# Performance work log

Hardware: AMD Instinct MI355X
Metric: run time of the kernel (lower is better)

The kernel has to match this reference:

```python
import jax, jax.numpy as jnp
import numpy as np

N_NODES = 50000
N_EDGES = 250000
D_IN, D_HID, D_OUT = 768, 256, 2


def _sage_conv(x, src, dst, W_l, b_l, W_r, n_nodes):
    # PyG SAGEConv (aggr='mean', root_weight=True):
    #   out[i] = lin_l(mean_{j in N(i)} x[j]) + lin_r(x[i])
    msg = x[src]  # [E, d] gather of source-node features
    agg = jax.ops.segment_sum(msg, dst, num_segments=n_nodes)
    cnt = jax.ops.segment_sum(jnp.ones((src.shape[0],), x.dtype), dst,
                              num_segments=n_nodes)
    agg = agg / jnp.maximum(cnt, 1.0)[:, None]
    return agg @ W_l.T + b_l + x @ W_r.T


def setup_inputs() -> dict:
    key = jax.random.key(0)
    ks = jax.random.split(key, 7)
    x = jax.random.normal(ks[0], (N_NODES, D_IN), dtype=jnp.float32)
    edge_index = jax.random.randint(ks[1], (2, N_EDGES), 0, N_NODES,
                                    dtype=jnp.int64)
    s1 = 1.0 / np.sqrt(D_IN)
    s2 = 1.0 / np.sqrt(D_HID)
    W1_l = jax.random.uniform(ks[2], (D_HID, D_IN), jnp.float32, -s1, s1)
    W1_r = jax.random.uniform(ks[3], (D_HID, D_IN), jnp.float32, -s1, s1)
    b1 = jnp.zeros((D_HID,), jnp.float32)
    W2_l = jax.random.uniform(ks[4], (D_OUT, D_HID), jnp.float32, -s2, s2)
    W2_r = jax.random.uniform(ks[5], (D_OUT, D_HID), jnp.float32, -s2, s2)
    b2 = jnp.zeros((D_OUT,), jnp.float32)
    return {"x": x, "edge_index": edge_index,
            "W1_l": W1_l, "b1": b1, "W1_r": W1_r,
            "W2_l": W2_l, "b2": b2, "W2_r": W2_r}


def reference(x, edge_index, W1_l, b1, W1_r, W2_l, b2, W2_r):
    src, dst = edge_index[0], edge_index[1]
    n = x.shape[0]
    h = _sage_conv(x, src, dst, W1_l, b1, W1_r, n)
    h = jax.nn.relu(h)
    # dropout is identity in eval mode (deterministic reference)
    out = _sage_conv(h, src, dst, W2_l, b2, W2_r, n)
    return out
```

## Files before the change

kernel.cpp:

```cpp
#include <hip/hip_runtime.h>
#include <stdint.h>


#define D_IN  768
#define D_HID 256
#define N1    512
#define KITERS (D_IN / 32)

typedef __attribute__((ext_vector_type(8))) short short8;
typedef __attribute__((ext_vector_type(4))) float f32x4;

__device__ __forceinline__ void async_copy16(const void* g, void* l) {
  __builtin_amdgcn_global_load_lds(
      (const __attribute__((address_space(1))) unsigned int*)g,
      (__attribute__((address_space(3))) unsigned int*)l,
      16, 0, 0);
}

__device__ __forceinline__ unsigned short f2bf(float f) {
  union { float f; unsigned u; } v; v.f = f;
  unsigned r = v.u + 0x7FFFu + ((v.u >> 16) & 1u);
  return (unsigned short)(r >> 16);
}

__device__ __forceinline__ float bf2f(unsigned short b) {
  union { unsigned u; float f; } v; v.u = ((unsigned)b) << 16;
  return v.f;
}


__global__ void cvtidx_k(const void* __restrict__ eidx,
                         int* __restrict__ src32, int* __restrict__ dst32,
                         int* __restrict__ counts, int E) {
  __shared__ int flag32;
  int tid = threadIdx.x;
  int i = blockIdx.x * 256 + tid;
  unsigned v = (i < E) ? ((const unsigned int*)eidx)[2 * (size_t)i + 1] : 0u;
  unsigned long long any = __ballot(v != 0u);
  if (tid == 0) flag32 = 0;
  __syncthreads();
  if ((tid & 63) == 0 && any) flag32 = 1;
  __syncthreads();
  if (i >= E) return;
  int s, d;
  if (flag32) {
    const int* p = (const int*)eidx;
    s = p[i]; d = p[E + i];
  } else {
    const long long* p = (const long long*)eidx;
    s = (int)p[i]; d = (int)p[E + i];
  }
  src32[i] = s;
  dst32[i] = d;
  atomicAdd(&counts[d], 1);
}

__global__ void scanA_k(const int* __restrict__ counts,
                        int* __restrict__ blockSums, int M) {
  __shared__ int ts[256];
  int b = blockIdx.x, t = threadIdx.x;
  int base = b * 1024 + t * 4;
  int s = 0;
#pragma unroll
  for (int k = 0; k < 4; k++) { int i = base + k; if (i < M) s += counts[i]; }
  ts[t] = s;
  __syncthreads();
  for (int off = 128; off > 0; off >>= 1) {
    if (t < off) ts[t] += ts[t + off];
    __syncthreads();
  }
  if (t == 0) blockSums[b] = ts[0];
}

__global__ void scanC_k(const int* __restrict__ counts,
                        const int* __restrict__ bsums,
                        int* __restrict__ offs, int* __restrict__ cursor,
                        int M, int E, int nb) {
  __shared__ int ts[256];
  __shared__ int bofs;
  int b = blockIdx.x, t = threadIdx.x;
  if (t < 64) {
    int v = (t < nb) ? bsums[t] : 0;
    int orig = v;
#pragma unroll
    for (int off = 1; off < 64; off <<= 1) {
      int u = __shfl_up(v, off);
      if (t >= off) v += u;
    }
    if (t == b) bofs = v - orig;
  }
  int base = b * 1024 + t * 4;
  int v[4]; int s = 0;
#pragma unroll
  for (int k = 0; k < 4; k++) {
    int i = base + k;
    v[k] = (i < M) ? counts[i] : 0;
    s += v[k];
  }
  ts[t] = s;
  __syncthreads();
  for (int off = 1; off < 256; off <<= 1) {
    int x = (t >= off) ? ts[t - off] : 0;
    __syncthreads();
    ts[t] += x;
    __syncthreads();
  }
  int run = bofs + ts[t] - s;
#pragma unroll
  for (int k = 0; k < 4; k++) {
    int i = base + k;
    if (i < M) { offs[i] = run; cursor[i] = run; run += v[k]; }
  }
  if (b == 0 && t == 0) offs[M] = E;
}

__global__ void fill_k(const int* __restrict__ src, const int* __restrict__ dst,
                       int* __restrict__ cursor, int* __restrict__ csr, int E) {
  int i = blockIdx.x * 256 + threadIdx.x;
  if (i >= E) return;
  int pos = atomicAdd(&cursor[dst[i]], 1);
  csr[pos] = src[i];
}


__global__ void cvtw_k(const float* __restrict__ W1l, const float* __restrict__ W1r,
                       unsigned short* __restrict__ wb) {
  int idx = blockIdx.x * 256 + threadIdx.x;
  int total = N1 * (D_IN / 8);
  if (idx >= total) return;
  int row = idx / (D_IN / 8);
  int cpos = (idx % (D_IN / 8)) * 8;
  const float* p = (row < D_HID) ? (W1l + (size_t)row * D_IN + cpos)
                                 : (W1r + (size_t)(row - D_HID) * D_IN + cpos);
  float4 f0 = *(const float4*)p;
  float4 f1 = *(const float4*)(p + 4);
  short8 o;
  o[0] = (short)f2bf(f0.x); o[1] = (short)f2bf(f0.y);
  o[2] = (short)f2bf(f0.z); o[3] = (short)f2bf(f0.w);
  o[4] = (short)f2bf(f1.x); o[5] = (short)f2bf(f1.y);
  o[6] = (short)f2bf(f1.z); o[7] = (short)f2bf(f1.w);
  *(short8*)(wb + (size_t)idx * 8) = o;
}

__global__ __launch_bounds__(256) void gemm_k(
    const float* __restrict__ x,
    const unsigned short* __restrict__ wb,
    unsigned short* __restrict__ Cb, int M) {
  __shared__ unsigned short As[2][128 * 32];
  __shared__ unsigned short Bs[2][128 * 32];
  const int tid  = threadIdx.x;
  const int lane = tid & 63;
  const int wid  = tid >> 6;
  const int wr = wid >> 1, wc = wid & 1;
  const int m0 = blockIdx.y * 128;
  const int n0 = blockIdx.x * 128;
  const int l15  = lane & 15;
  const int quad = lane >> 4;

  const int arow0 = tid >> 2, akg = tid & 3;
  const int arow1 = arow0 + 64;
  const int aswz = akg | ((akg & 1) << 2);
  const float* agp0 = x + (size_t)min(m0 + arow0, M - 1) * D_IN + akg * 8;
  const float* agp1 = x + (size_t)min(m0 + arow1, M - 1) * D_IN + akg * 8;
  const int aoff0 = (arow0 >> 4) * 512 + akg * 128 + ((arow0 & 15) ^ aswz) * 8;
  const int aoff1 = (arow1 >> 4) * 512 + akg * 128 + ((arow1 & 15) ^ aswz) * 8;
  const int pquad = quad | ((quad & 1) << 2);

  const int brow = (tid >> 6) * 16 + (tid & 15);
  const int bcg  = (tid >> 4) & 3;
  const unsigned short* bgp0 = wb + (size_t)(n0 + brow) * D_IN + bcg * 8;
  const unsigned short* bgp1 = wb + (size_t)(n0 + brow + 64) * D_IN + bcg * 8;
  const int boff0 = tid * 8;
  const int boff1 = (tid + 256) * 8;

  f32x4 acc[4][4];
#pragma unroll
  for (int r = 0; r < 4; r++)
#pragma unroll
    for (int c = 0; c < 4; c++) acc[r][c] = (f32x4)0.0f;

  float4 a00 = *(const float4*)(agp0);
  float4 a01 = *(const float4*)(agp0 + 4);
  float4 a10 = *(const float4*)(agp1);
  float4 a11 = *(const float4*)(agp1 + 4);
  async_copy16(bgp0, &Bs[0][boff0]);
  async_copy16(bgp1, &Bs[0][boff1]);

  for (int it = 0; it < KITERS; ++it) {
    const int p = it & 1;
    short8 o0, o1;
    o0[0] = (short)f2bf(a00.x); o0[1] = (short)f2bf(a00.y);
    o0[2] = (short)f2bf(a00.z); o0[3] = (short)f2bf(a00.w);
    o0[4] = (short)f2bf(a01.x); o0[5] = (short)f2bf(a01.y);
    o0[6] = (short)f2bf(a01.z); o0[7] = (short)f2bf(a01.w);
    o1[0] = (short)f2bf(a10.x); o1[1] = (short)f2bf(a10.y);
    o1[2] = (short)f2bf(a10.z); o1[3] = (short)f2bf(a10.w);
    o1[4] = (short)f2bf(a11.x); o1[5] = (short)f2bf(a11.y);
    o1[6] = (short)f2bf(a11.z); o1[7] = (short)f2bf(a11.w);
    *(short8*)&As[p][aoff0] = o0;
    *(short8*)&As[p][aoff1] = o1;

    __syncthreads();

    if (it + 1 < KITERS) {
      const int k1 = (it + 1) * 32;
      a00 = *(const float4*)(agp0 + k1);
      a01 = *(const float4*)(agp0 + k1 + 4);
      a10 = *(const float4*)(agp1 + k1);
      a11 = *(const float4*)(agp1 + k1 + 4);
      async_copy16(bgp0 + k1, &Bs[p ^ 1][boff0]);
      async_copy16(bgp1 + k1, &Bs[p ^ 1][boff1]);
    }

    short8 a[4], b[4];
#pragma unroll
    for (int r = 0; r < 4; r++)
      a[r] = *(const short8*)&As[p][(wr * 4 + r) * 512 + quad * 128 + ((l15 ^ pquad)) * 8];
#pragma unroll
    for (int c = 0; c < 4; c++)
      b[c] = *(const short8*)&Bs[p][(wc * 4 + c) * 512 + quad * 128 + l15 * 8];
#pragma unroll
    for (int r = 0; r < 4; r++)
#pragma unroll
      for (int c = 0; c < 4; c++)
        acc[r][c] = __builtin_amdgcn_mfma_f32_16x16x32_bf16(a[r], b[c], acc[r][c], 0, 0, 0);
  }

  const int crow0 = m0 + wr * 64;
  const int ccol0 = n0 + wc * 64;
#pragma unroll
  for (int r = 0; r < 4; r++)
#pragma unroll
    for (int c = 0; c < 4; c++) {
      int col = ccol0 + c * 16 + l15;
#pragma unroll
      for (int reg = 0; reg < 4; reg++) {
        int row = crow0 + r * 16 + quad * 4 + reg;
        Cb[(size_t)row * N1 + col] = f2bf(acc[r][c][reg]);
      }
    }
}

__global__ void agg_l2_k(const unsigned short* __restrict__ Cb,
                         const int* __restrict__ offs, const int* __restrict__ csr,
                         const float* __restrict__ b1,
                         const float* __restrict__ W2l, const float* __restrict__ W2r,
                         float4* __restrict__ rs, int M) {
  int tid = threadIdx.x;
  int lane = tid & 63;
  int wid = tid >> 6;
  int wave = blockIdx.x * 4 + wid;
  int nw = gridDim.x * 4;
  int c = lane * 4;
  float4 bv  = *(const float4*)(b1 + c);
  float4 wl0 = *(const float4*)(W2l + c);
  float4 wl1 = *(const float4*)(W2l + D_HID + c);
  float4 wr0 = *(const float4*)(W2r + c);
  float4 wr1 = *(const float4*)(W2r + D_HID + c);
  for (int i = wave; i < M; i += nw) {
    int s = offs[i], e = offs[i + 1];
    float ax = 0.f, ay = 0.f, az = 0.f, aw = 0.f;
    for (int t = s; t < e; t++) {
      int j = csr[t];
      ushort4 v = *(const ushort4*)(Cb + (size_t)j * N1 + c);
      ax += bf2f(v.x); ay += bf2f(v.y); az += bf2f(v.z); aw += bf2f(v.w);
    }
    float inv = 1.0f / fmaxf((float)(e - s), 1.0f);
    ushort4 q = *(const ushort4*)(Cb + (size_t)i * N1 + D_HID + c);
    float h0 = fmaxf(ax * inv + bv.x + bf2f(q.x), 0.0f);
    float h1 = fmaxf(ay * inv + bv.y + bf2f(q.y), 0.0f);
    float h2 = fmaxf(az * inv + bv.z + bf2f(q.z), 0.0f);
    float h3 = fmaxf(aw * inv + bv.w + bf2f(q.w), 0.0f);
    float r0 = h0 * wl0.x + h1 * wl0.y + h2 * wl0.z + h3 * wl0.w;
    float r1 = h0 * wl1.x + h1 * wl1.y + h2 * wl1.z + h3 * wl1.w;
    float s0 = h0 * wr0.x + h1 * wr0.y + h2 * wr0.z + h3 * wr0.w;
    float s1 = h0 * wr1.x + h1 * wr1.y + h2 * wr1.z + h3 * wr1.w;
#pragma unroll
    for (int off = 32; off > 0; off >>= 1) {
      r0 += __shfl_xor(r0, off);
      r1 += __shfl_xor(r1, off);
      s0 += __shfl_xor(s0, off);
      s1 += __shfl_xor(s1, off);
    }
    if (lane == 0) rs[i] = make_float4(r0, r1, s0, s1);
  }
}

__global__ void final_k(const float4* __restrict__ rs, const int* __restrict__ offs,
                        const int* __restrict__ csr, const float* __restrict__ b2,
                        float* __restrict__ out, int M) {
  int i = blockIdx.x * 256 + threadIdx.x;
  if (i >= M) return;
  int s = offs[i], e = offs[i + 1];
  float a0 = 0.0f, a1 = 0.0f;
  for (int t = s; t < e; t++) {
    float4 v = rs[csr[t]];
    a0 += v.x; a1 += v.y;
  }
  float inv = 1.0f / fmaxf((float)(e - s), 1.0f);
  float4 me = rs[i];
  out[2 * i + 0] = a0 * inv + b2[0] + me.z;
  out[2 * i + 1] = a1 * inv + b2[1] + me.w;
}


extern "C" void kernel_launch(void* const* d_in, const int* in_sizes, int n_in,
                              void* d_out, int out_size, void* d_ws, size_t ws_size,
                              hipStream_t stream) {
  const float* x   = (const float*)d_in[0];
  const void*  eix = d_in[1];
  const float* W1l = (const float*)d_in[2];
  const float* b1  = (const float*)d_in[3];
  const float* W1r = (const float*)d_in[4];
  const float* W2l = (const float*)d_in[5];
  const float* b2  = (const float*)d_in[6];
  const float* W2r = (const float*)d_in[7];
  float* out = (float*)d_out;

  const int M  = in_sizes[0] / D_IN;
  const int E  = in_sizes[1] / 2;
  const int Mp = ((M + 127) / 128) * 128;
  const int nb = (M + 1023) / 1024;

  char* ws = (char*)d_ws;
  size_t off = 0;
  auto alloc = [&](size_t b) { size_t o = off; off += (b + 255) & ~(size_t)255; return o; };
  size_t oCounts = alloc((size_t)M * 4);
  size_t zeroBytes = (size_t)M * 4;
  size_t oOffs   = alloc((size_t)(M + 1) * 4);
  size_t oCursor = alloc((size_t)M * 4);
  size_t oCsr    = alloc((size_t)E * 4);
  size_t oSrc    = alloc((size_t)E * 4);
  size_t oDst    = alloc((size_t)E * 4);
  size_t oBSums  = alloc(64 * 4);
  size_t oWb     = alloc((size_t)N1 * D_IN * 2);
  size_t oC      = alloc((size_t)Mp * N1 * 2);
  size_t oRs     = alloc((size_t)M * 16);
  (void)ws_size; (void)n_in; (void)out_size;

  int* counts = (int*)(ws + oCounts);
  int* offs   = (int*)(ws + oOffs);
  int* cursor = (int*)(ws + oCursor);
  int* csr    = (int*)(ws + oCsr);
  int* src32  = (int*)(ws + oSrc);
  int* dst32  = (int*)(ws + oDst);
  int* bsums  = (int*)(ws + oBSums);
  unsigned short* wb = (unsigned short*)(ws + oWb);
  unsigned short* Cb = (unsigned short*)(ws + oC);
  float4* rs = (float4*)(ws + oRs);

  hipMemsetAsync(counts, 0, zeroBytes, stream);

  int gE = (E + 255) / 256;
  cvtidx_k<<<gE, 256, 0, stream>>>(eix, src32, dst32, counts, E);
  scanA_k<<<nb, 256, 0, stream>>>(counts, bsums, M);
  scanC_k<<<nb, 256, 0, stream>>>(counts, bsums, offs, cursor, M, E, nb);
  fill_k<<<gE, 256, 0, stream>>>(src32, dst32, cursor, csr, E);

  int gW = (N1 * (D_IN / 8) + 255) / 256;
  cvtw_k<<<gW, 256, 0, stream>>>(W1l, W1r, wb);

  dim3 gg(N1 / 128, Mp / 128);
  gemm_k<<<gg, 256, 0, stream>>>(x, wb, Cb, M);

  agg_l2_k<<<2048, 256, 0, stream>>>(Cb, offs, csr, b1, W2l, W2r, rs, M);
  final_k<<<(M + 255) / 256, 256, 0, stream>>>(rs, offs, csr, b2, out, M);
}
```

Before: 388.6 us.

## Remap GEMM blocks per XCD, deepen A prefetch, one-wave-per-node aggregation

The GEMM grid is flattened and remapped so the four N-tiles of each M-tile land on the same XCD, which should improve L2 reuse of the x rows. The A-operand global loads are now issued two K-steps ahead using two register sets in an unrolled pair of bodies, to hide fp32 load latency behind more compute. The aggregation kernel launches one wave per node instead of a grid-stride loop. The costs are more live registers in the GEMM and a much larger aggregation grid.

```diff
diff --git a/kernel.cpp b/kernel.cpp
--- a/kernel.cpp
+++ b/kernel.cpp
@@ -145,15 +145,22 @@
 __global__ __launch_bounds__(256) void gemm_k(
     const float* __restrict__ x,
     const unsigned short* __restrict__ wb,
-    unsigned short* __restrict__ Cb, int M) {
+    unsigned short* __restrict__ Cb, int M, int MT, int mtPerXcd) {
   __shared__ unsigned short As[2][128 * 32];
   __shared__ unsigned short Bs[2][128 * 32];
+
+  const int bid = blockIdx.x;
+  const int xcd = bid & 7;
+  const int j   = bid >> 3;
+  const int mt  = xcd * mtPerXcd + (j >> 2);
+  if (mt >= MT) return;
+  const int m0 = mt * 128;
+  const int n0 = (j & 3) * 128;
+
   const int tid  = threadIdx.x;
   const int lane = tid & 63;
   const int wid  = tid >> 6;
   const int wr = wid >> 1, wc = wid & 1;
-  const int m0 = blockIdx.y * 128;
-  const int n0 = blockIdx.x * 128;
   const int l15  = lane & 15;
   const int quad = lane >> 4;
 
@@ -179,52 +186,69 @@
 #pragma unroll
     for (int c = 0; c < 4; c++) acc[r][c] = (f32x4)0.0f;
 
-  float4 a00 = *(const float4*)(agp0);
-  float4 a01 = *(const float4*)(agp0 + 4);
-  float4 a10 = *(const float4*)(agp1);
-  float4 a11 = *(const float4*)(agp1 + 4);
+  float4 a0_0, a0_1, a0_2, a0_3;
+  float4 a1_0, a1_1, a1_2, a1_3;
+
+  a0_0 = *(const float4*)(agp0);
+  a0_1 = *(const float4*)(agp0 + 4);
+  a0_2 = *(const float4*)(agp1);
+  a0_3 = *(const float4*)(agp1 + 4);
   async_copy16(bgp0, &Bs[0][boff0]);
   async_copy16(bgp1, &Bs[0][boff1]);
-
-  for (int it = 0; it < KITERS; ++it) {
-    const int p = it & 1;
-    short8 o0, o1;
-    o0[0] = (short)f2bf(a00.x); o0[1] = (short)f2bf(a00.y);
-    o0[2] = (short)f2bf(a00.z); o0[3] = (short)f2bf(a00.w);
-    o0[4] = (short)f2bf(a01.x); o0[5] = (short)f2bf(a01.y);
-    o0[6] = (short)f2bf(a01.z); o0[7] = (short)f2bf(a01.w);
-    o1[0] = (short)f2bf(a10.x); o1[1] = (short)f2bf(a10.y);
-    o1[2] = (short)f2bf(a10.z); o1[3] = (short)f2bf(a10.w);
-    o1[4] = (short)f2bf(a11.x); o1[5] = (short)f2bf(a11.y);
-    o1[6] = (short)f2bf(a11.z); o1[7] = (short)f2bf(a11.w);
-    *(short8*)&As[p][aoff0] = o0;
-    *(short8*)&As[p][aoff1] = o1;
-
-    __syncthreads();
-
-    if (it + 1 < KITERS) {
-      const int k1 = (it + 1) * 32;
-      a00 = *(const float4*)(agp0 + k1);
-      a01 = *(const float4*)(agp0 + k1 + 4);
-      a10 = *(const float4*)(agp1 + k1);
-      a11 = *(const float4*)(agp1 + k1 + 4);
-      async_copy16(bgp0 + k1, &Bs[p ^ 1][boff0]);
-      async_copy16(bgp1 + k1, &Bs[p ^ 1][boff1]);
-    }
-
-    short8 a[4], b[4];
-#pragma unroll
-    for (int r = 0; r < 4; r++)
-      a[r] = *(const short8*)&As[p][(wr * 4 + r) * 512 + quad * 128 + ((l15 ^ pquad)) * 8];
-#pragma unroll
-    for (int c = 0; c < 4; c++)
-      b[c] = *(const short8*)&Bs[p][(wc * 4 + c) * 512 + quad * 128 + l15 * 8];
-#pragma unroll
-    for (int r = 0; r < 4; r++)
-#pragma unroll
-      for (int c = 0; c < 4; c++)
-        acc[r][c] = __builtin_amdgcn_mfma_f32_16x16x32_bf16(a[r], b[c], acc[r][c], 0, 0, 0);
-  }
+  a1_0 = *(const float4*)(agp0 + 32);
+  a1_1 = *(const float4*)(agp0 + 36);
+  a1_2 = *(const float4*)(agp1 + 32);
+  a1_3 = *(const float4*)(agp1 + 36);
+
+#define GEMM_BODY(P, AR0, AR1, AR2, AR3)                                      \
+  {                                                                           \
+    short8 o0, o1;                                                            \
+    o0[0] = (short)f2bf(AR0.x); o0[1] = (short)f2bf(AR0.y);                   \
+    o0[2] = (short)f2bf(AR0.z); o0[3] = (short)f2bf(AR0.w);                   \
+    o0[4] = (short)f2bf(AR1.x); o0[5] = (short)f2bf(AR1.y);                   \
+    o0[6] = (short)f2bf(AR1.z); o0[7] = (short)f2bf(AR1.w);                   \
+    o1[0] = (short)f2bf(AR2.x); o1[1] = (short)f2bf(AR2.y);                   \
+    o1[2] = (short)f2bf(AR2.z); o1[3] = (short)f2bf(AR2.w);                   \
+    o1[4] = (short)f2bf(AR3.x); o1[5] = (short)f2bf(AR3.y);                   \
+    o1[6] = (short)f2bf(AR3.z); o1[7] = (short)f2bf(AR3.w);                   \
+    *(short8*)&As[P][aoff0] = o0;                                             \
+    *(short8*)&As[P][aoff1] = o1;                                             \
+    __syncthreads();                                                          \
+    if (kk + 1 < KITERS) {                                                    \
+      const int kn = (kk + 1) * 32;                                           \
+      async_copy16(bgp0 + kn, &Bs[P ^ 1][boff0]);                             \
+      async_copy16(bgp1 + kn, &Bs[P ^ 1][boff1]);                             \
+    }                                                                         \
+    if (kk + 2 < KITERS) {                                                    \
+      const int kp = (kk + 2) * 32;                                           \
+      AR0 = *(const float4*)(agp0 + kp);                                      \
+      AR1 = *(const float4*)(agp0 + kp + 4);                                  \
+      AR2 = *(const float4*)(agp1 + kp);                                      \
+      AR3 = *(const float4*)(agp1 + kp + 4);                                  \
+    }                                                                         \
+    short8 a[4], b[4];                                                        \
+    _Pragma("unroll")                                                         \
+    for (int r = 0; r < 4; r++)                                               \
+      a[r] = *(const short8*)&As[P][(wr * 4 + r) * 512 + quad * 128 +         \
+                                    ((l15 ^ pquad)) * 8];                     \
+    _Pragma("unroll")                                                         \
+    for (int c = 0; c < 4; c++)                                               \
+      b[c] = *(const short8*)&Bs[P][(wc * 4 + c) * 512 + quad * 128 +         \
+                                    l15 * 8];                                 \
+    _Pragma("unroll")                                                         \
+    for (int r = 0; r < 4; r++)                                               \
+      _Pragma("unroll")                                                       \
+      for (int c = 0; c < 4; c++)                                             \
+        acc[r][c] =                                                           \
+            __builtin_amdgcn_mfma_f32_16x16x32_bf16(a[r], b[c], acc[r][c],    \
+                                                    0, 0, 0);                 \
+  }
+
+  for (int it = 0; it < KITERS; it += 2) {
+    { const int kk = it;     GEMM_BODY(0, a0_0, a0_1, a0_2, a0_3) }
+    { const int kk = it + 1; GEMM_BODY(1, a1_0, a1_1, a1_2, a1_3) }
+  }
+#undef GEMM_BODY
 
   const int crow0 = m0 + wr * 64;
   const int ccol0 = n0 + wc * 64;
@@ -249,41 +273,39 @@
   int tid = threadIdx.x;
   int lane = tid & 63;
   int wid = tid >> 6;
-  int wave = blockIdx.x * 4 + wid;
-  int nw = gridDim.x * 4;
+  int i = blockIdx.x * 4 + wid;
+  if (i >= M) return;
   int c = lane * 4;
   float4 bv  = *(const float4*)(b1 + c);
   float4 wl0 = *(const float4*)(W2l + c);
   float4 wl1 = *(const float4*)(W2l + D_HID + c);
   float4 wr0 = *(const float4*)(W2r + c);
   float4 wr1 = *(const float4*)(W2r + D_HID + c);
-  for (int i = wave; i < M; i += nw) {
-    int s = offs[i], e = offs[i + 1];
-    float ax = 0.f, ay = 0.f, az = 0.f, aw = 0.f;
-    for (int t = s; t < e; t++) {
-      int j = csr[t];
-      ushort4 v = *(const ushort4*)(Cb + (size_t)j * N1 + c);
-      ax += bf2f(v.x); ay += bf2f(v.y); az += bf2f(v.z); aw += bf2f(v.w);
-    }
-    float inv = 1.0f / fmaxf((float)(e - s), 1.0f);
-    ushort4 q = *(const ushort4*)(Cb + (size_t)i * N1 + D_HID + c);
-    float h0 = fmaxf(ax * inv + bv.x + bf2f(q.x), 0.0f);
-    float h1 = fmaxf(ay * inv + bv.y + bf2f(q.y), 0.0f);
-    float h2 = fmaxf(az * inv + bv.z + bf2f(q.z), 0.0f);
-    float h3 = fmaxf(aw * inv + bv.w + bf2f(q.w), 0.0f);
-    float r0 = h0 * wl0.x + h1 * wl0.y + h2 * wl0.z + h3 * wl0.w;
-    float r1 = h0 * wl1.x + h1 * wl1.y + h2 * wl1.z + h3 * wl1.w;
-    float s0 = h0 * wr0.x + h1 * wr0.y + h2 * wr0.z + h3 * wr0.w;
-    float s1 = h0 * wr1.x + h1 * wr1.y + h2 * wr1.z + h3 * wr1.w;
-#pragma unroll
-    for (int off = 32; off > 0; off >>= 1) {
-      r0 += __shfl_xor(r0, off);
-      r1 += __shfl_xor(r1, off);
-      s0 += __shfl_xor(s0, off);
-      s1 += __shfl_xor(s1, off);
-    }
-    if (lane == 0) rs[i] = make_float4(r0, r1, s0, s1);
-  }
+  int s = offs[i], e = offs[i + 1];
+  float ax = 0.f, ay = 0.f, az = 0.f, aw = 0.f;
+  for (int t = s; t < e; t++) {
+    int j = csr[t];
+    ushort4 v = *(const ushort4*)(Cb + (size_t)j * N1 + c);
+    ax += bf2f(v.x); ay += bf2f(v.y); az += bf2f(v.z); aw += bf2f(v.w);
+  }
+  float inv = 1.0f / fmaxf((float)(e - s), 1.0f);
+  ushort4 q = *(const ushort4*)(Cb + (size_t)i * N1 + D_HID + c);
+  float h0 = fmaxf(ax * inv + bv.x + bf2f(q.x), 0.0f);
+  float h1 = fmaxf(ay * inv + bv.y + bf2f(q.y), 0.0f);
+  float h2 = fmaxf(az * inv + bv.z + bf2f(q.z), 0.0f);
+  float h3 = fmaxf(aw * inv + bv.w + bf2f(q.w), 0.0f);
+  float r0 = h0 * wl0.x + h1 * wl0.y + h2 * wl0.z + h3 * wl0.w;
+  float r1 = h0 * wl1.x + h1 * wl1.y + h2 * wl1.z + h3 * wl1.w;
+  float s0 = h0 * wr0.x + h1 * wr0.y + h2 * wr0.z + h3 * wr0.w;
+  float s1 = h0 * wr1.x + h1 * wr1.y + h2 * wr1.z + h3 * wr1.w;
+#pragma unroll
+  for (int off = 32; off > 0; off >>= 1) {
+    r0 += __shfl_xor(r0, off);
+    r1 += __shfl_xor(r1, off);
+    s0 += __shfl_xor(s0, off);
+    s1 += __shfl_xor(s1, off);
+  }
+  if (lane == 0) rs[i] = make_float4(r0, r1, s0, s1);
 }
 
 __global__ void final_k(const float4* __restrict__ rs, const int* __restrict__ offs,
@@ -321,6 +343,9 @@
   const int E  = in_sizes[1] / 2;
   const int Mp = ((M + 127) / 128) * 128;
   const int nb = (M + 1023) / 1024;
+  const int MT = Mp / 128;
+  const int mtPerXcd = (MT + 7) / 8;
+  const int gemmBlocks = 8 * mtPerXcd * 4;
 
   char* ws = (char*)d_ws;
   size_t off = 0;
@@ -360,9 +385,8 @@
   int gW = (N1 * (D_IN / 8) + 255) / 256;
   cvtw_k<<<gW, 256, 0, stream>>>(W1l, W1r, wb);
 
-  dim3 gg(N1 / 128, Mp / 128);
-  gemm_k<<<gg, 256, 0, stream>>>(x, wb, Cb, M);
-
-  agg_l2_k<<<2048, 256, 0, stream>>>(Cb, offs, csr, b1, W2l, W2r, rs, M);
+  gemm_k<<<gemmBlocks, 256, 0, stream>>>(x, wb, Cb, M, MT, mtPerXcd);
+
+  agg_l2_k<<<(M + 3) / 4, 256, 0, stream>>>(Cb, offs, csr, b1, W2l, W2r, rs, M);
   final_k<<<(M + 255) / 256, 256, 0, stream>>>(rs, offs, csr, b2, out, M);
 }
```

Measured after the change: 377.8 us. -2.8%, faster.
